# Kernel optimization log

Measured on AMD Instinct MI355X. Metric: run time of the kernel, lower is better.

The kernel has to match this reference:

```python
import jax, jax.numpy as jnp
import numpy as np

EPS = 1e-5

def _layernorm(x, g, b):
    mu = jnp.mean(x, axis=-1, keepdims=True)
    var = jnp.mean(jnp.square(x - mu), axis=-1, keepdims=True)
    return (x - mu) * jax.lax.rsqrt(var + EPS) * g + b

def _silu(x):
    return x * jax.nn.sigmoid(x)

def _xavier(key, shape):
    fan_out, fan_in = shape
    limit = np.sqrt(6.0 / (fan_in + fan_out))
    return jax.random.uniform(key, shape, jnp.float32, -limit, limit)

def setup_inputs() -> dict:
    key = jax.random.key(0)
    ks = jax.random.split(key, 4)
    B = 2097152
    return {
        'x': jax.random.normal(ks[0], (B, 24), jnp.float32),
        'w1': _xavier(ks[1], (64, 24)), 'b1': jnp.zeros((64,), jnp.float32),
        'g1': jnp.ones((64,), jnp.float32), 'be1': jnp.zeros((64,), jnp.float32),
        'w2': _xavier(ks[2], (64, 64)), 'b2': jnp.zeros((64,), jnp.float32),
        'g2': jnp.ones((64,), jnp.float32), 'be2': jnp.zeros((64,), jnp.float32),
        'w3': _xavier(ks[3], (7, 64)), 'b3': jnp.zeros((7,), jnp.float32),
        'g3': jnp.ones((7,), jnp.float32), 'be3': jnp.zeros((7,), jnp.float32),
    }

def reference(x, w1, b1, g1, be1, w2, b2, g2, be2, w3, b3, g3, be3):
    h = _silu(_layernorm(x @ w1.T + b1, g1, be1))      # [B, 64]
    h = _silu(_layernorm(h @ w2.T + b2, g2, be2))      # [B, 64]
    h = _layernorm(h @ w3.T + b3, g3, be3)             # [B, 7]
    return jax.nn.softmax(h, axis=-1)
```

## Files before the change

### kernel.cpp

```cpp
#include <hip/hip_runtime.h>
#include <math.h>

#define BLOCK 256
#define WPB 4
#define NBLOCKS 2048

typedef float  f32x4 __attribute__((ext_vector_type(4)));
typedef float  f32x2 __attribute__((ext_vector_type(2)));
typedef short  short8 __attribute__((ext_vector_type(8)));
typedef unsigned int u32;
typedef u32 u32x4 __attribute__((ext_vector_type(4)));
typedef u32 u32x2 __attribute__((ext_vector_type(2)));

static __device__ __forceinline__ f32x4 mfma16(short8 a, short8 b, f32x4 c) {
    return __builtin_amdgcn_mfma_f32_16x16x32_bf16(a, b, c, 0, 0, 0);
}

static __device__ __forceinline__ u32 cvt_pk(float lo, float hi) {
    u32 r;
    asm("v_cvt_pk_bf16_f32 %0, %1, %2" : "=v"(r) : "v"(lo), "v"(hi));
    return r;
}
static __device__ __forceinline__ float unpk_lo(u32 p) { return __builtin_bit_cast(float, p << 16); }
static __device__ __forceinline__ float unpk_hi(u32 p) { return __builtin_bit_cast(float, p & 0xffff0000u); }

static __device__ __forceinline__ short8 mk_frag(u32 a, u32 b, u32 c, u32 d) {
    u32x4 t = {a, b, c, d};
    return __builtin_bit_cast(short8, t);
}

struct Frag2 { short8 hi, lo; };

static __device__ __forceinline__ Frag2 split8(f32x4 a, f32x4 b) {
    u32 h0 = cvt_pk(a[0], a[1]), h1 = cvt_pk(a[2], a[3]);
    u32 h2 = cvt_pk(b[0], b[1]), h3 = cvt_pk(b[2], b[3]);
    u32 l0 = cvt_pk(a[0] - unpk_lo(h0), a[1] - unpk_hi(h0));
    u32 l1 = cvt_pk(a[2] - unpk_lo(h1), a[3] - unpk_hi(h1));
    u32 l2 = cvt_pk(b[0] - unpk_lo(h2), b[1] - unpk_hi(h2));
    u32 l3 = cvt_pk(b[2] - unpk_lo(h3), b[3] - unpk_hi(h3));
    Frag2 r; r.hi = mk_frag(h0, h1, h2, h3); r.lo = mk_frag(l0, l1, l2, l3);
    return r;
}

static __device__ __forceinline__ void split4(f32x4 v, u32x2& hi, u32x2& lo) {
    u32 h0 = cvt_pk(v[0], v[1]), h1 = cvt_pk(v[2], v[3]);
    u32 l0 = cvt_pk(v[0] - unpk_lo(h0), v[1] - unpk_hi(h0));
    u32 l1 = cvt_pk(v[2] - unpk_lo(h1), v[3] - unpk_hi(h1));
    hi = u32x2{h0, h1}; lo = u32x2{l0, l1};
}

static __device__ __forceinline__ Frag2 wfrag(const float* p) {
    return split8(*(const f32x4*)p, *(const f32x4*)(p + 4));
}

static __device__ __forceinline__ float red4(float v) {
    v += __shfl_xor(v, 16);
    v += __shfl_xor(v, 32);
    return v;
}
static __device__ __forceinline__ float redmax4(float v) {
    v = fmaxf(v, __shfl_xor(v, 16));
    v = fmaxf(v, __shfl_xor(v, 32));
    return v;
}

__global__ __launch_bounds__(BLOCK, 2) void mlp_mfma_kernel(
    const float* __restrict__ x,
    const float* __restrict__ w1, const float* __restrict__ b1,
    const float* __restrict__ g1, const float* __restrict__ be1,
    const float* __restrict__ w2, const float* __restrict__ b2,
    const float* __restrict__ g2, const float* __restrict__ be2,
    const float* __restrict__ w3, const float* __restrict__ b3,
    const float* __restrict__ g3, const float* __restrict__ be3,
    float* __restrict__ out, int ntiles)
{
    __shared__ __align__(16) unsigned char smem[WPB * 4096 + WPB * 768];
    __shared__ __align__(16) float sP[6 * 64 + 3 * 16];

    const int tid = threadIdx.x;
    const int lane = tid & 63;
    const int wib  = tid >> 6;
    const int c = lane & 15;
    const int q = lane >> 4;

    if (tid < 64) {
        sP[        tid] = b1[tid];  sP[ 64 + tid] = g1[tid];  sP[128 + tid] = be1[tid];
        sP[192 + tid] = b2[tid];    sP[256 + tid] = g2[tid];  sP[320 + tid] = be2[tid];
    }
    if (tid < 16) {
        const bool ok = tid < 7;
        sP[384 + tid] = ok ? b3[tid]  : 0.f;
        sP[400 + tid] = ok ? g3[tid]  : 0.f;
        sP[416 + tid] = ok ? be3[tid] : 0.f;
    }

    unsigned char* sHi   = smem + wib * 4096;
    unsigned char* sLo   = sHi + 2048;
    unsigned char* obase = smem + WPB * 4096 + wib * 768;

    const u32 crow = (u32)c * 128u;
    const u32 ch   = (u32)(c & 7);

    const f32x4 z4 = {0.f, 0.f, 0.f, 0.f};

    Frag2 w1f[4];
#pragma unroll
    for (int mt = 0; mt < 4; ++mt) {
        if (q < 3) {
            w1f[mt] = wfrag(w1 + (mt * 16 + c) * 24 + q * 8);
        } else {
            float s = b1[mt * 16 + c];
            f32x4 a = {s, 0.f, 0.f, 0.f};
            w1f[mt] = split8(a, z4);
        }
    }
    Frag2 w2f[4][2];
#pragma unroll
    for (int mt = 0; mt < 4; ++mt)
#pragma unroll
        for (int kk = 0; kk < 2; ++kk)
            w2f[mt][kk] = wfrag(w2 + (mt * 16 + c) * 64 + kk * 32 + q * 8);
    Frag2 w3f[2];
#pragma unroll
    for (int kk = 0; kk < 2; ++kk) {
        if (c < 7) w3f[kk] = wfrag(w3 + c * 64 + kk * 32 + q * 8);
        else       w3f[kk] = split8(z4, z4);
    }

    __syncthreads();

    const int c0 = lane / 7, f0 = lane - c0 * 7;
    const int i1 = lane + 64;
    const int c1 = i1 / 7, f1 = i1 - c1 * 7;

    const int wid = blockIdx.x * WPB + wib;
    const int tstride = gridDim.x * WPB;

    f32x4 xa = z4, xb = z4;
    int tile = wid;
    if (tile < ntiles && q < 3) {
        const float* xp = x + ((size_t)tile * 16 + c) * 24 + q * 8;
        xa = *(const f32x4*)xp;
        xb = *(const f32x4*)(xp + 4);
    }
    if (q == 3) xa[0] = 1.0f;

    for (; tile < ntiles; tile += tstride) {
        asm volatile("" ::: "memory");

        Frag2 bx = split8(xa, xb);

        {
            const int nt = tile + tstride;
            if (nt < ntiles && q < 3) {
                const float* xp = x + ((size_t)nt * 16 + c) * 24 + q * 8;
                xa = *(const f32x4*)xp;
                xb = *(const f32x4*)(xp + 4);
            }
        }

        f32x4 d1[4];
#pragma unroll
        for (int mt = 0; mt < 4; ++mt) {
            f32x4 d = mfma16(w1f[mt].hi, bx.hi, z4);
            d = mfma16(w1f[mt].hi, bx.lo, d);
            d = mfma16(w1f[mt].lo, bx.hi, d);
            d1[mt] = d;
        }
        {
            float s = 0.f, s2 = 0.f;
#pragma unroll
            for (int mt = 0; mt < 4; ++mt)
#pragma unroll
                for (int r = 0; r < 4; ++r) {
                    float v = d1[mt][r];
                    s += v; s2 = fmaf(v, v, s2);
                }
            s = red4(s); s2 = red4(s2);
            const float mu = s * (1.f / 64.f);
            const float var = s2 * (1.f / 64.f) - mu * mu;
            const float inv = __builtin_amdgcn_rsqf(var + 1e-5f);
#pragma unroll
            for (int mt = 0; mt < 4; ++mt) {
                const f32x4 gv  = *(const f32x4*)(sP +  64 + mt * 16 + q * 4);
                const f32x4 bev = *(const f32x4*)(sP + 128 + mt * 16 + q * 4);
#pragma unroll
                for (int r = 0; r < 4; ++r) {
                    float t = (d1[mt][r] - mu) * inv;
                    float v = fmaf(t, gv[r], bev[r]);
                    d1[mt][r] = v * __builtin_amdgcn_rcpf(1.f + __expf(-v));
                }
            }
        }

#pragma unroll
        for (int mt = 0; mt < 4; ++mt) {
            u32x2 hi, lo;
            split4(d1[mt], hi, lo);
            u32 off = crow + ((((u32)(mt * 2 + (q >> 1))) ^ ch) << 4) + (u32)((q & 1) * 8);
            *(u32x2*)(sHi + off) = hi;
            *(u32x2*)(sLo + off) = lo;
        }
        short8 bhHi[2], bhLo[2];
#pragma unroll
        for (int kk = 0; kk < 2; ++kk) {
            u32 roff = crow + ((((u32)(kk * 4 + q)) ^ ch) << 4);
            bhHi[kk] = *(const short8*)(sHi + roff);
            bhLo[kk] = *(const short8*)(sLo + roff);
        }

        f32x4 d2[4];
#pragma unroll
        for (int mt = 0; mt < 4; ++mt) {
            f32x4 d = mfma16(w2f[mt][0].hi, bhHi[0], z4);
            d = mfma16(w2f[mt][0].hi, bhLo[0], d);
            d = mfma16(w2f[mt][0].lo, bhHi[0], d);
            d = mfma16(w2f[mt][1].hi, bhHi[1], d);
            d = mfma16(w2f[mt][1].hi, bhLo[1], d);
            d = mfma16(w2f[mt][1].lo, bhHi[1], d);
            d2[mt] = d;
        }
        {
            float s = 0.f, s2 = 0.f;
#pragma unroll
            for (int mt = 0; mt < 4; ++mt) {
                const f32x4 bv = *(const f32x4*)(sP + 192 + mt * 16 + q * 4);
#pragma unroll
                for (int r = 0; r < 4; ++r) {
                    float v = d2[mt][r] + bv[r];
                    d2[mt][r] = v;
                    s += v; s2 = fmaf(v, v, s2);
                }
            }
            s = red4(s); s2 = red4(s2);
            const float mu = s * (1.f / 64.f);
            const float var = s2 * (1.f / 64.f) - mu * mu;
            const float inv = __builtin_amdgcn_rsqf(var + 1e-5f);
#pragma unroll
            for (int mt = 0; mt < 4; ++mt) {
                const f32x4 gv  = *(const f32x4*)(sP + 256 + mt * 16 + q * 4);
                const f32x4 bev = *(const f32x4*)(sP + 320 + mt * 16 + q * 4);
#pragma unroll
                for (int r = 0; r < 4; ++r) {
                    float t = (d2[mt][r] - mu) * inv;
                    float v = fmaf(t, gv[r], bev[r]);
                    d2[mt][r] = v * __builtin_amdgcn_rcpf(1.f + __expf(-v));
                }
            }
        }

#pragma unroll
        for (int mt = 0; mt < 4; ++mt) {
            u32x2 hi, lo;
            split4(d2[mt], hi, lo);
            u32 off = crow + ((((u32)(mt * 2 + (q >> 1))) ^ ch) << 4) + (u32)((q & 1) * 8);
            *(u32x2*)(sHi + off) = hi;
            *(u32x2*)(sLo + off) = lo;
        }
#pragma unroll
        for (int kk = 0; kk < 2; ++kk) {
            u32 roff = crow + ((((u32)(kk * 4 + q)) ^ ch) << 4);
            bhHi[kk] = *(const short8*)(sHi + roff);
            bhLo[kk] = *(const short8*)(sLo + roff);
        }

        f32x4 d3a = mfma16(w3f[0].hi, bhHi[0], z4);
        d3a = mfma16(w3f[0].hi, bhLo[0], d3a);
        d3a = mfma16(w3f[0].lo, bhHi[0], d3a);
        f32x4 d3b = mfma16(w3f[1].hi, bhHi[1], z4);
        d3b = mfma16(w3f[1].hi, bhLo[1], d3b);
        d3b = mfma16(w3f[1].lo, bhHi[1], d3b);
        f32x4 d3;
#pragma unroll
        for (int r = 0; r < 4; ++r) d3[r] = d3a[r] + d3b[r];

        {
            const f32x4 b3v  = *(const f32x4*)(sP + 384 + q * 4);
            const f32x4 g3v  = *(const f32x4*)(sP + 400 + q * 4);
            const f32x4 be3v = *(const f32x4*)(sP + 416 + q * 4);
            float s = 0.f, s2 = 0.f;
#pragma unroll
            for (int r = 0; r < 4; ++r) {
                float v = d3[r] + b3v[r];
                d3[r] = v;
                const bool ok = (q * 4 + r) < 7;
                if (ok) { s += v; s2 = fmaf(v, v, s2); }
            }
            s = red4(s); s2 = red4(s2);
            const float mu = s * (1.f / 7.f);
            const float var = s2 * (1.f / 7.f) - mu * mu;
            const float inv = __builtin_amdgcn_rsqf(var + 1e-5f);

            float z[4]; float mx = -1e30f;
#pragma unroll
            for (int r = 0; r < 4; ++r) {
                z[r] = fmaf((d3[r] - mu) * inv, g3v[r], be3v[r]);
                const bool ok = (q * 4 + r) < 7;
                if (ok) mx = fmaxf(mx, z[r]);
            }
            mx = redmax4(mx);
            float es = 0.f; float e[4];
#pragma unroll
            for (int r = 0; r < 4; ++r) {
                const bool ok = (q * 4 + r) < 7;
                e[r] = ok ? __expf(z[r] - mx) : 0.f;
                es += e[r];
            }
            es = red4(es);
            const float rs = __builtin_amdgcn_rcpf(es);

            if (q == 0) {
                f32x4 v = {e[0] * rs, e[1] * rs, e[2] * rs, e[3] * rs};
                *(f32x4*)(obase + c * 48) = v;
            } else if (q == 1) {
                f32x2 v = {e[0] * rs, e[1] * rs};
                *(f32x2*)(obase + c * 48 + 16) = v;
                *(float*)(obase + c * 48 + 24) = e[2] * rs;
            }
            float* outp = out + (size_t)tile * 112;
            float r0 = *(const float*)(obase + c0 * 48 + f0 * 4);
            outp[lane] = r0;
            if (lane < 48) {
                float r1 = *(const float*)(obase + c1 * 48 + f1 * 4);
                outp[64 + lane] = r1;
            }
        }
    }
}

extern "C" void kernel_launch(void* const* d_in, const int* in_sizes, int n_in,
                              void* d_out, int out_size, void* d_ws, size_t ws_size,
                              hipStream_t stream) {
    const float* x   = (const float*)d_in[0];
    const float* w1  = (const float*)d_in[1];
    const float* b1  = (const float*)d_in[2];
    const float* g1  = (const float*)d_in[3];
    const float* be1 = (const float*)d_in[4];
    const float* w2  = (const float*)d_in[5];
    const float* b2  = (const float*)d_in[6];
    const float* g2  = (const float*)d_in[7];
    const float* be2 = (const float*)d_in[8];
    const float* w3  = (const float*)d_in[9];
    const float* b3  = (const float*)d_in[10];
    const float* g3  = (const float*)d_in[11];
    const float* be3 = (const float*)d_in[12];
    float* out = (float*)d_out;

    const int B = in_sizes[0] / 24;
    const int ntiles = B / 16;
    hipLaunchKernelGGL(mlp_mfma_kernel, dim3(NBLOCKS), dim3(BLOCK), 0, stream,
                       x, w1, b1, g1, be1, w2, b2, g2, be2, w3, b3, g3, be3,
                       out, ntiles);
}
```

Measured before the change: 220.8 us.

## Interleave two independent tiles per wave to overlap MFMA and VALU phases

Each wave now processes two 16-row tiles (A and B) per iteration, interleaving their layer phases so one tile's MFMA chain can overlap the other tile's layernorm/SiLU math and LDS staging. LDS staging buffers are doubled per wave and the x prefetch covers two tiles ahead. This aims to hide MFMA and dependency latency through instruction-level parallelism, at the cost of higher register pressure under launch_bounds(256,2) and more shared memory, which risks spills or lower occupancy.

```diff
diff --git a/kernel.cpp b/kernel.cpp
--- a/kernel.cpp
+++ b/kernel.cpp
@@ -15,6 +15,8 @@
 static __device__ __forceinline__ f32x4 mfma16(short8 a, short8 b, f32x4 c) {
     return __builtin_amdgcn_mfma_f32_16x16x32_bf16(a, b, c, 0, 0, 0);
 }
+
+static __device__ __forceinline__ f32x4 zero4() { f32x4 z = {0.f, 0.f, 0.f, 0.f}; return z; }
 
 static __device__ __forceinline__ u32 cvt_pk(float lo, float hi) {
     u32 r;
@@ -64,7 +66,151 @@
     return v;
 }
 
-__global__ __launch_bounds__(BLOCK, 2) void mlp_mfma_kernel(
+struct TState {
+    f32x4 xa, xb;
+    f32x4 d[4];
+    short8 bhHi[2], bhLo[2];
+    f32x4 d3;
+};
+
+static __device__ __forceinline__ void ph_l1(TState& t, const Frag2& bx, const Frag2* w1f) {
+#pragma unroll
+    for (int mt = 0; mt < 4; ++mt) {
+        f32x4 d = mfma16(w1f[mt].hi, bx.hi, zero4());
+        d = mfma16(w1f[mt].hi, bx.lo, d);
+        d = mfma16(w1f[mt].lo, bx.hi, d);
+        t.d[mt] = d;
+    }
+}
+
+static __device__ __forceinline__ void ph_l2(TState& t, const Frag2 (*w2f)[2]) {
+#pragma unroll
+    for (int mt = 0; mt < 4; ++mt) {
+        f32x4 d = mfma16(w2f[mt][0].hi, t.bhHi[0], zero4());
+        d = mfma16(w2f[mt][0].hi, t.bhLo[0], d);
+        d = mfma16(w2f[mt][0].lo, t.bhHi[0], d);
+        d = mfma16(w2f[mt][1].hi, t.bhHi[1], d);
+        d = mfma16(w2f[mt][1].hi, t.bhLo[1], d);
+        d = mfma16(w2f[mt][1].lo, t.bhHi[1], d);
+        t.d[mt] = d;
+    }
+}
+
+static __device__ __forceinline__ void ph_l3(TState& t, const Frag2* w3f) {
+    f32x4 a = mfma16(w3f[0].hi, t.bhHi[0], zero4());
+    a = mfma16(w3f[0].hi, t.bhLo[0], a);
+    a = mfma16(w3f[0].lo, t.bhHi[0], a);
+    f32x4 b = mfma16(w3f[1].hi, t.bhHi[1], zero4());
+    b = mfma16(w3f[1].hi, t.bhLo[1], b);
+    b = mfma16(w3f[1].lo, t.bhHi[1], b);
+#pragma unroll
+    for (int r = 0; r < 4; ++r) t.d3[r] = a[r] + b[r];
+}
+
+template<int PB, int PG, int PBE>
+static __device__ __forceinline__ void ph_ln_silu(TState& t, const float* sP, int q) {
+    float s = 0.f, s2 = 0.f;
+#pragma unroll
+    for (int mt = 0; mt < 4; ++mt) {
+        if (PB >= 0) {
+            const f32x4 bv = *(const f32x4*)(sP + PB + mt * 16 + q * 4);
+#pragma unroll
+            for (int r = 0; r < 4; ++r) t.d[mt][r] += bv[r];
+        }
+#pragma unroll
+        for (int r = 0; r < 4; ++r) { float v = t.d[mt][r]; s += v; s2 = fmaf(v, v, s2); }
+    }
+    s = red4(s); s2 = red4(s2);
+    const float mu = s * (1.f / 64.f);
+    const float var = s2 * (1.f / 64.f) - mu * mu;
+    const float inv = __builtin_amdgcn_rsqf(var + 1e-5f);
+    const float cns = -mu * inv;
+#pragma unroll
+    for (int mt = 0; mt < 4; ++mt) {
+        const f32x4 gv  = *(const f32x4*)(sP + PG  + mt * 16 + q * 4);
+        const f32x4 bev = *(const f32x4*)(sP + PBE + mt * 16 + q * 4);
+#pragma unroll
+        for (int r = 0; r < 4; ++r) {
+            float tt = fmaf(t.d[mt][r], inv, cns);
+            float v  = fmaf(tt, gv[r], bev[r]);
+            t.d[mt][r] = v * __builtin_amdgcn_rcpf(1.f + __expf(-v));
+        }
+    }
+}
+
+static __device__ __forceinline__ void ph_stage(TState& t, unsigned char* sHi, unsigned char* sLo,
+                                                u32 crow, u32 ch, int q) {
+#pragma unroll
+    for (int mt = 0; mt < 4; ++mt) {
+        u32x2 hi, lo;
+        split4(t.d[mt], hi, lo);
+        u32 off = crow + ((((u32)(mt * 2 + (q >> 1))) ^ ch) << 4) + (u32)((q & 1) * 8);
+        *(u32x2*)(sHi + off) = hi;
+        *(u32x2*)(sLo + off) = lo;
+    }
+#pragma unroll
+    for (int kk = 0; kk < 2; ++kk) {
+        u32 roff = crow + ((((u32)(kk * 4 + q)) ^ ch) << 4);
+        t.bhHi[kk] = *(const short8*)(sHi + roff);
+        t.bhLo[kk] = *(const short8*)(sLo + roff);
+    }
+}
+
+static __device__ __forceinline__ void ph_out(TState& t, const float* sP, int q, int c, int lane,
+                                              unsigned char* ob, float* out, int tile, bool valid,
+                                              int oc0, int of0, int oc1, int of1) {
+    const f32x4 b3v  = *(const f32x4*)(sP + 384 + q * 4);
+    const f32x4 g3v  = *(const f32x4*)(sP + 400 + q * 4);
+    const f32x4 be3v = *(const f32x4*)(sP + 416 + q * 4);
+    f32x4 d3 = t.d3;
+    float s = 0.f, s2 = 0.f;
+#pragma unroll
+    for (int r = 0; r < 4; ++r) {
+        float v = d3[r] + b3v[r];
+        d3[r] = v;
+        const bool ok = (q * 4 + r) < 7;
+        if (ok) { s += v; s2 = fmaf(v, v, s2); }
+    }
+    s = red4(s); s2 = red4(s2);
+    const float mu = s * (1.f / 7.f);
+    const float var = s2 * (1.f / 7.f) - mu * mu;
+    const float inv = __builtin_amdgcn_rsqf(var + 1e-5f);
+    const float cns = -mu * inv;
+
+    float z[4]; float mx = -1e30f;
+#pragma unroll
+    for (int r = 0; r < 4; ++r) {
+        z[r] = fmaf(fmaf(d3[r], inv, cns), g3v[r], be3v[r]);
+        const bool ok = (q * 4 + r) < 7;
+        if (ok) mx = fmaxf(mx, z[r]);
+    }
+    mx = redmax4(mx);
+    float es = 0.f; float e[4];
+#pragma unroll
+    for (int r = 0; r < 4; ++r) {
+        const bool ok = (q * 4 + r) < 7;
+        e[r] = ok ? __expf(z[r] - mx) : 0.f;
+        es += e[r];
+    }
+    es = red4(es);
+    const float rs = __builtin_amdgcn_rcpf(es);
+
+    if (q == 0) {
+        f32x4 v = {e[0] * rs, e[1] * rs, e[2] * rs, e[3] * rs};
+        *(f32x4*)(ob + c * 48) = v;
+    } else if (q == 1) {
+        f32x2 v = {e[0] * rs, e[1] * rs};
+        *(f32x2*)(ob + c * 48 + 16) = v;
+        *(float*)(ob + c * 48 + 24) = e[2] * rs;
+    }
+    if (valid) {
+        float* outp = out + (size_t)tile * 112;
+        outp[lane] = *(const float*)(ob + oc0 * 48 + of0 * 4);
+        if (lane < 48) outp[64 + lane] = *(const float*)(ob + oc1 * 48 + of1 * 4);
+    }
+}
+
+__global__ __launch_bounds__(BLOCK, 2) void mlp_mfma2_kernel(
     const float* __restrict__ x,
     const float* __restrict__ w1, const float* __restrict__ b1,
     const float* __restrict__ g1, const float* __restrict__ be1,
@@ -74,7 +220,7 @@
     const float* __restrict__ g3, const float* __restrict__ be3,
     float* __restrict__ out, int ntiles)
 {
-    __shared__ __align__(16) unsigned char smem[WPB * 4096 + WPB * 768];
+    __shared__ __align__(16) unsigned char smem[WPB * (2 * 4096 + 2 * 768)];
     __shared__ __align__(16) float sP[6 * 64 + 3 * 16];
 
     const int tid = threadIdx.x;
@@ -94,14 +240,16 @@
         sP[416 + tid] = ok ? be3[tid] : 0.f;
     }
 
-    unsigned char* sHi   = smem + wib * 4096;
-    unsigned char* sLo   = sHi + 2048;
-    unsigned char* obase = smem + WPB * 4096 + wib * 768;
+    unsigned char* wb   = smem + wib * (2 * 4096 + 2 * 768);
+    unsigned char* sHiA = wb;
+    unsigned char* sLoA = wb + 2048;
+    unsigned char* sHiB = wb + 4096;
+    unsigned char* sLoB = wb + 6144;
+    unsigned char* obA  = wb + 8192;
+    unsigned char* obB  = wb + 8960;
 
     const u32 crow = (u32)c * 128u;
     const u32 ch   = (u32)(c & 7);
-
-    const f32x4 z4 = {0.f, 0.f, 0.f, 0.f};
 
     Frag2 w1f[4];
 #pragma unroll
@@ -111,7 +259,7 @@
         } else {
             float s = b1[mt * 16 + c];
             f32x4 a = {s, 0.f, 0.f, 0.f};
-            w1f[mt] = split8(a, z4);
+            w1f[mt] = split8(a, zero4());
         }
     }
     Frag2 w2f[4][2];
@@ -124,207 +272,63 @@
 #pragma unroll
     for (int kk = 0; kk < 2; ++kk) {
         if (c < 7) w3f[kk] = wfrag(w3 + c * 64 + kk * 32 + q * 8);
-        else       w3f[kk] = split8(z4, z4);
+        else       { w3f[kk].hi = mk_frag(0,0,0,0); w3f[kk].lo = mk_frag(0,0,0,0); }
     }
 
     __syncthreads();
 
-    const int c0 = lane / 7, f0 = lane - c0 * 7;
+    const int oc0 = lane / 7, of0 = lane - oc0 * 7;
     const int i1 = lane + 64;
-    const int c1 = i1 / 7, f1 = i1 - c1 * 7;
+    const int oc1 = i1 / 7, of1 = i1 - oc1 * 7;
 
     const int wid = blockIdx.x * WPB + wib;
-    const int tstride = gridDim.x * WPB;
-
-    f32x4 xa = z4, xb = z4;
-    int tile = wid;
-    if (tile < ntiles && q < 3) {
-        const float* xp = x + ((size_t)tile * 16 + c) * 24 + q * 8;
-        xa = *(const f32x4*)xp;
-        xb = *(const f32x4*)(xp + 4);
-    }
-    if (q == 3) xa[0] = 1.0f;
-
-    for (; tile < ntiles; tile += tstride) {
+    const int ts  = gridDim.x * WPB;
+
+    TState A, B;
+    A.xa = zero4(); A.xb = zero4(); B.xa = zero4(); B.xb = zero4();
+    {
+        const int t0 = wid, t1 = wid + ts;
+        if (t0 < ntiles && q < 3) {
+            const float* xp = x + ((size_t)t0 * 16 + c) * 24 + q * 8;
+            A.xa = *(const f32x4*)xp; A.xb = *(const f32x4*)(xp + 4);
+        }
+        if (t1 < ntiles && q < 3) {
+            const float* xp = x + ((size_t)t1 * 16 + c) * 24 + q * 8;
+            B.xa = *(const f32x4*)xp; B.xb = *(const f32x4*)(xp + 4);
+        }
+        if (q == 3) { A.xa[0] = 1.0f; B.xa[0] = 1.0f; }
+    }
+
+    for (int tile = wid; tile < ntiles; tile += 2 * ts) {
         asm volatile("" ::: "memory");
 
-        Frag2 bx = split8(xa, xb);
+        const int tB = tile + ts;
+        const bool vB = tB < ntiles;
+
+        Frag2 bxA = split8(A.xa, A.xb);
+        Frag2 bxB = split8(B.xa, B.xb);
 
         {
-            const int nt = tile + tstride;
-            if (nt < ntiles && q < 3) {
-                const float* xp = x + ((size_t)nt * 16 + c) * 24 + q * 8;
-                xa = *(const f32x4*)xp;
-                xb = *(const f32x4*)(xp + 4);
+            const int tA2 = tile + 2 * ts, tB2 = tile + 3 * ts;
+            if (tA2 < ntiles && q < 3) {
+                const float* xp = x + ((size_t)tA2 * 16 + c) * 24 + q * 8;
+                A.xa = *(const f32x4*)xp; A.xb = *(const f32x4*)(xp + 4);
             }
-        }
-
-        f32x4 d1[4];
-#pragma unroll
-        for (int mt = 0; mt < 4; ++mt) {
-            f32x4 d = mfma16(w1f[mt].hi, bx.hi, z4);
-            d = mfma16(w1f[mt].hi, bx.lo, d);
-            d = mfma16(w1f[mt].lo, bx.hi, d);
-            d1[mt] = d;
-        }
-        {
-            float s = 0.f, s2 = 0.f;
-#pragma unroll
-            for (int mt = 0; mt < 4; ++mt)
-#pragma unroll
-                for (int r = 0; r < 4; ++r) {
-                    float v = d1[mt][r];
-                    s += v; s2 = fmaf(v, v, s2);
-                }
-            s = red4(s); s2 = red4(s2);
-            const float mu = s * (1.f / 64.f);
-            const float var = s2 * (1.f / 64.f) - mu * mu;
-            const float inv = __builtin_amdgcn_rsqf(var + 1e-5f);
-#pragma unroll
-            for (int mt = 0; mt < 4; ++mt) {
-                const f32x4 gv  = *(const f32x4*)(sP +  64 + mt * 16 + q * 4);
-                const f32x4 bev = *(const f32x4*)(sP + 128 + mt * 16 + q * 4);
-#pragma unroll
-                for (int r = 0; r < 4; ++r) {
-                    float t = (d1[mt][r] - mu) * inv;
-                    float v = fmaf(t, gv[r], bev[r]);
-                    d1[mt][r] = v * __builtin_amdgcn_rcpf(1.f + __expf(-v));
-                }
+            if (tB2 < ntiles && q < 3) {
+                const float* xp = x + ((size_t)tB2 * 16 + c) * 24 + q * 8;
+                B.xa = *(const f32x4*)xp; B.xb = *(const f32x4*)(xp + 4);
             }
         }
 
-#pragma unroll
-        for (int mt = 0; mt < 4; ++mt) {
-            u32x2 hi, lo;
-            split4(d1[mt], hi, lo);
-            u32 off = crow + ((((u32)(mt * 2 + (q >> 1))) ^ ch) << 4) + (u32)((q & 1) * 8);
-            *(u32x2*)(sHi + off) = hi;
-            *(u32x2*)(sLo + off) = lo;
-        }
-        short8 bhHi[2], bhLo[2];
-#pragma unroll
-        for (int kk = 0; kk < 2; ++kk) {
-            u32 roff = crow + ((((u32)(kk * 4 + q)) ^ ch) << 4);
-            bhHi[kk] = *(const short8*)(sHi + roff);
-            bhLo[kk] = *(const short8*)(sLo + roff);
-        }
-
-        f32x4 d2[4];
-#pragma unroll
-        for (int mt = 0; mt < 4; ++mt) {
-            f32x4 d = mfma16(w2f[mt][0].hi, bhHi[0], z4);
-            d = mfma16(w2f[mt][0].hi, bhLo[0], d);
-            d = mfma16(w2f[mt][0].lo, bhHi[0], d);
-            d = mfma16(w2f[mt][1].hi, bhHi[1], d);
-            d = mfma16(w2f[mt][1].hi, bhLo[1], d);
-            d = mfma16(w2f[mt][1].lo, bhHi[1], d);
-            d2[mt] = d;
-        }
-        {
-            float s = 0.f, s2 = 0.f;
-#pragma unroll
-            for (int mt = 0; mt < 4; ++mt) {
-                const f32x4 bv = *(const f32x4*)(sP + 192 + mt * 16 + q * 4);
-#pragma unroll
-                for (int r = 0; r < 4; ++r) {
-                    float v = d2[mt][r] + bv[r];
-                    d2[mt][r] = v;
-                    s += v; s2 = fmaf(v, v, s2);
-                }
-            }
-            s = red4(s); s2 = red4(s2);
-            const float mu = s * (1.f / 64.f);
-            const float var = s2 * (1.f / 64.f) - mu * mu;
-            const float inv = __builtin_amdgcn_rsqf(var + 1e-5f);
-#pragma unroll
-            for (int mt = 0; mt < 4; ++mt) {
-                const f32x4 gv  = *(const f32x4*)(sP + 256 + mt * 16 + q * 4);
-                const f32x4 bev = *(const f32x4*)(sP + 320 + mt * 16 + q * 4);
-#pragma unroll
-                for (int r = 0; r < 4; ++r) {
-                    float t = (d2[mt][r] - mu) * inv;
-                    float v = fmaf(t, gv[r], bev[r]);
-                    d2[mt][r] = v * __builtin_amdgcn_rcpf(1.f + __expf(-v));
-                }
-            }
-        }
-
-#pragma unroll
-        for (int mt = 0; mt < 4; ++mt) {
-            u32x2 hi, lo;
-            split4(d2[mt], hi, lo);
-            u32 off = crow + ((((u32)(mt * 2 + (q >> 1))) ^ ch) << 4) + (u32)((q & 1) * 8);
-            *(u32x2*)(sHi + off) = hi;
-            *(u32x2*)(sLo + off) = lo;
-        }
-#pragma unroll
-        for (int kk = 0; kk < 2; ++kk) {
-            u32 roff = crow + ((((u32)(kk * 4 + q)) ^ ch) << 4);
-            bhHi[kk] = *(const short8*)(sHi + roff);
-            bhLo[kk] = *(const short8*)(sLo + roff);
-        }
-
-        f32x4 d3a = mfma16(w3f[0].hi, bhHi[0], z4);
-        d3a = mfma16(w3f[0].hi, bhLo[0], d3a);
-        d3a = mfma16(w3f[0].lo, bhHi[0], d3a);
-        f32x4 d3b = mfma16(w3f[1].hi, bhHi[1], z4);
-        d3b = mfma16(w3f[1].hi, bhLo[1], d3b);
-        d3b = mfma16(w3f[1].lo, bhHi[1], d3b);
-        f32x4 d3;
-#pragma unroll
-        for (int r = 0; r < 4; ++r) d3[r] = d3a[r] + d3b[r];
-
-        {
-            const f32x4 b3v  = *(const f32x4*)(sP + 384 + q * 4);
-            const f32x4 g3v  = *(const f32x4*)(sP + 400 + q * 4);
-            const f32x4 be3v = *(const f32x4*)(sP + 416 + q * 4);
-            float s = 0.f, s2 = 0.f;
-#pragma unroll
-            for (int r = 0; r < 4; ++r) {
-                float v = d3[r] + b3v[r];
-                d3[r] = v;
-                const bool ok = (q * 4 + r) < 7;
-                if (ok) { s += v; s2 = fmaf(v, v, s2); }
-            }
-            s = red4(s); s2 = red4(s2);
-            const float mu = s * (1.f / 7.f);
-            const float var = s2 * (1.f / 7.f) - mu * mu;
-            const float inv = __builtin_amdgcn_rsqf(var + 1e-5f);
-
-            float z[4]; float mx = -1e30f;
-#pragma unroll
-            for (int r = 0; r < 4; ++r) {
-                z[r] = fmaf((d3[r] - mu) * inv, g3v[r], be3v[r]);
-                const bool ok = (q * 4 + r) < 7;
-                if (ok) mx = fmaxf(mx, z[r]);
-            }
-            mx = redmax4(mx);
-            float es = 0.f; float e[4];
-#pragma unroll
-            for (int r = 0; r < 4; ++r) {
-                const bool ok = (q * 4 + r) < 7;
-                e[r] = ok ? __expf(z[r] - mx) : 0.f;
-                es += e[r];
-            }
-            es = red4(es);
-            const float rs = __builtin_amdgcn_rcpf(es);
-
-            if (q == 0) {
-                f32x4 v = {e[0] * rs, e[1] * rs, e[2] * rs, e[3] * rs};
-                *(f32x4*)(obase + c * 48) = v;
-            } else if (q == 1) {
-                f32x2 v = {e[0] * rs, e[1] * rs};
-                *(f32x2*)(obase + c * 48 + 16) = v;
-                *(float*)(obase + c * 48 + 24) = e[2] * rs;
-            }
-            float* outp = out + (size_t)tile * 112;
-            float r0 = *(const float*)(obase + c0 * 48 + f0 * 4);
-            outp[lane] = r0;
-            if (lane < 48) {
-                float r1 = *(const float*)(obase + c1 * 48 + f1 * 4);
-                outp[64 + lane] = r1;
-            }
-        }
+        ph_l1(A, bxA, w1f);                 ph_l1(B, bxB, w1f);
+        ph_ln_silu<-1, 64, 128>(A, sP, q);  ph_ln_silu<-1, 64, 128>(B, sP, q);
+        ph_stage(A, sHiA, sLoA, crow, ch, q); ph_stage(B, sHiB, sLoB, crow, ch, q);
+        ph_l2(A, w2f);                      ph_l2(B, w2f);
+        ph_ln_silu<192, 256, 320>(A, sP, q); ph_ln_silu<192, 256, 320>(B, sP, q);
+        ph_stage(A, sHiA, sLoA, crow, ch, q); ph_stage(B, sHiB, sLoB, crow, ch, q);
+        ph_l3(A, w3f);                      ph_l3(B, w3f);
+        ph_out(A, sP, q, c, lane, obA, out, tile, true, oc0, of0, oc1, of1);
+        ph_out(B, sP, q, c, lane, obB, out, tB,   vB,   oc0, of0, oc1, of1);
     }
 }
 
@@ -348,7 +352,7 @@
 
     const int B = in_sizes[0] / 24;
     const int ntiles = B / 16;
-    hipLaunchKernelGGL(mlp_mfma_kernel, dim3(NBLOCKS), dim3(BLOCK), 0, stream,
+    hipLaunchKernelGGL(mlp_mfma2_kernel, dim3(NBLOCKS), dim3(BLOCK), 0, stream,
                        x, w1, b1, g1, be1, w2, b2, g2, be2, w3, b3, g3, be3,
                        out, ntiles);
 }
```

Measured after the change: 200.7 us. 1.1x faster.
